# Kernel tuning notes

Hardware: AMD Instinct MI355X
Metric: run time of the kernel (lower is better)

The kernel has to match this reference:

```python
import jax, jax.numpy as jnp
import numpy as np

UNIT1 = 16384
UNITS = 3 * UNIT1          # self.units = unit1 * 3
INPUT_DIM = 15             # pinned by goal/color/pos/act segment lengths
BATCH = 2048


def _make_mask():
    """Reproduce the per-unit diagonal connectivity masks as a dense [UNITS, INPUT_DIM]
    0/1 matrix (the diagonal of each unit's s[u] matrix).
    Probabilities match np.random.randint thresholds in the original:
      group1 (u < unit1):        cols 0:3 -> 1, 3:6 -> P=2/5, 6:9 -> P=1/10, 9:15 -> 0
      group2 (unit1..2*unit1):   cols 0:3 -> P=5/10, 3:6 -> P=4/5, 6:9 -> P=3/5, 9:15 -> P=2/10
      group3 (2*unit1..3*unit1): cols 0:3 -> 0, 3:6 -> P=1/5, 6:9 -> 1, 9:15 -> 1
    """
    rng = np.random.default_rng(0)

    def block(n, specs):
        cols = []
        for width, p in specs:
            if p <= 0.0:
                cols.append(np.zeros((n, width), np.float32))
            elif p >= 1.0:
                cols.append(np.ones((n, width), np.float32))
            else:
                cols.append((rng.random((n, width)) < p).astype(np.float32))
        return np.concatenate(cols, axis=1)

    g1 = block(UNIT1, [(3, 1.0), (3, 0.4), (3, 0.1), (6, 0.0)])
    g2 = block(UNIT1, [(3, 0.5), (3, 0.8), (3, 0.6), (6, 0.2)])
    g3 = block(UNIT1, [(3, 0.0), (3, 0.2), (3, 1.0), (6, 1.0)])
    return np.concatenate([g1, g2, g3], axis=0)  # [UNITS, INPUT_DIM]


def setup_inputs() -> dict:
    key = jax.random.key(0)
    k_x, k_w = jax.random.split(key)
    inputs = jax.random.normal(k_x, (BATCH, INPUT_DIM), dtype=jnp.float32)
    # w_init = uniform(0, 0.01); non_neg constraint is satisfied at init
    w = jax.random.uniform(k_w, (INPUT_DIM, UNITS), dtype=jnp.float32,
                           minval=0.0, maxval=0.01)
    # b_init = uniform(0, 0) == zeros
    b = jnp.zeros((UNITS,), dtype=jnp.float32)
    mask = jnp.asarray(_make_mask())  # [UNITS, INPUT_DIM], structural constant
    return {"inputs": inputs, "w": w, "b": b, "mask": mask}


def reference(inputs, w, b, mask):
    # Original: p = (s @ inputs^T)^T -> [B, U, D]; f = diag(p @ w) + b -> [B, U].
    # Since s[u] = diag(mask[u]):
    #   f[b, u] = sum_i inputs[b, i] * mask[u, i] * w[i, u] + b[u]
    # i.e. a dense GEMM with the elementwise-masked weight matrix.
    masked_w = w * mask.T                    # [D, U]
    return inputs @ masked_w + b             # [B, U]
```

## Files before the change

### kernel.cpp

```cpp
#include <hip/hip_runtime.h>

#define UNITS     49152
#define INPUT_DIM 15
#define BATCH     2048

constexpr int TPB            = 256;
constexpr int U_PER_THREAD   = 4;
constexpr int U_PER_BLOCK    = TPB * U_PER_THREAD;
constexpr int ROWS_PER_BLOCK = 32;

typedef float f32x4 __attribute__((ext_vector_type(4)));

__global__ __launch_bounds__(TPB) void premask_kernel(
    const float* __restrict__ w,
    const float* __restrict__ mask,
    float* __restrict__ mw)
{
    const int u = blockIdx.x * TPB + threadIdx.x;
    float m[INPUT_DIM];
#pragma unroll
    for (int i = 0; i < INPUT_DIM; ++i) m[i] = mask[(size_t)u * INPUT_DIM + i];
#pragma unroll
    for (int i = 0; i < INPUT_DIM; ++i)
        mw[(size_t)i * UNITS + u] = w[(size_t)i * UNITS + u] * m[i];
}

template <bool PREMASKED>
__global__ __launch_bounds__(TPB) void striatum_kernel(
    const float* __restrict__ x,
    const float* __restrict__ w,
    const float* __restrict__ bias,
    const float* __restrict__ mask,
    float* __restrict__ out)
{
    __shared__ float xs[ROWS_PER_BLOCK * INPUT_DIM];

    const int u0   = blockIdx.x * U_PER_BLOCK + threadIdx.x * U_PER_THREAD;
    const int row0 = blockIdx.y * ROWS_PER_BLOCK;

    for (int idx = threadIdx.x; idx < ROWS_PER_BLOCK * INPUT_DIM; idx += TPB) {
        xs[idx] = x[row0 * INPUT_DIM + idx];
    }

    f32x4 mw[INPUT_DIM];
#pragma unroll
    for (int i = 0; i < INPUT_DIM; ++i) {
        f32x4 wv = *reinterpret_cast<const f32x4*>(&w[(size_t)i * UNITS + u0]);
        if constexpr (!PREMASKED) {
            wv.x *= mask[(size_t)(u0 + 0) * INPUT_DIM + i];
            wv.y *= mask[(size_t)(u0 + 1) * INPUT_DIM + i];
            wv.z *= mask[(size_t)(u0 + 2) * INPUT_DIM + i];
            wv.w *= mask[(size_t)(u0 + 3) * INPUT_DIM + i];
        }
        mw[i] = wv;
    }
    const f32x4 bv = *reinterpret_cast<const f32x4*>(&bias[u0]);

    __syncthreads();

    for (int r = 0; r < ROWS_PER_BLOCK; ++r) {
        const float* xr = &xs[r * INPUT_DIM];
        f32x4 acc = bv;
#pragma unroll
        for (int i = 0; i < INPUT_DIM; ++i) {
            const float xv = xr[i];
            acc.x = fmaf(xv, mw[i].x, acc.x);
            acc.y = fmaf(xv, mw[i].y, acc.y);
            acc.z = fmaf(xv, mw[i].z, acc.z);
            acc.w = fmaf(xv, mw[i].w, acc.w);
        }
        *reinterpret_cast<f32x4*>(&out[(size_t)(row0 + r) * UNITS + u0]) = acc;
    }
}

extern "C" void kernel_launch(void* const* d_in, const int* in_sizes, int n_in,
                              void* d_out, int out_size, void* d_ws, size_t ws_size,
                              hipStream_t stream) {
    const float* x    = (const float*)d_in[0];
    const float* w    = (const float*)d_in[1];
    const float* b    = (const float*)d_in[2];
    const float* mask = (const float*)d_in[3];
    float* out        = (float*)d_out;

    dim3 grid(UNITS / U_PER_BLOCK, BATCH / ROWS_PER_BLOCK);
    const size_t mw_bytes = (size_t)INPUT_DIM * UNITS * sizeof(float);

    if (ws_size >= mw_bytes) {
        float* mw = (float*)d_ws;
        premask_kernel<<<UNITS / TPB, TPB, 0, stream>>>(w, mask, mw);
        striatum_kernel<true><<<grid, TPB, 0, stream>>>(x, mw, b, mask, out);
    } else {
        striatum_kernel<false><<<grid, TPB, 0, stream>>>(x, w, b, mask, out);
    }
}
```

Before: 86.91 us.

## Reshape grid to fewer larger blocks, vectorize x loads, nontemporal stores

Changes the block size to 384 threads and the grid to 32 column blocks by 8 row groups of 256 rows each, so every block reuses its register-resident masked weights across many more rows. The shared x tile is padded to a stride of 16 so rows can be read as float4, and four rows are processed per iteration. Output is written with nontemporal stores, since the output is a large write-only stream. The grid shrinks to 256 blocks, which may underfill the GPU's compute units and lengthen the per-block tail.

After: 94.40 us. 8.6% more time.

```diff
diff --git a/kernel.cpp b/kernel.cpp
--- a/kernel.cpp
+++ b/kernel.cpp
@@ -4,19 +4,23 @@
 #define INPUT_DIM 15
 #define BATCH     2048
 
-constexpr int TPB            = 256;
+constexpr int TPB            = 384;
 constexpr int U_PER_THREAD   = 4;
 constexpr int U_PER_BLOCK    = TPB * U_PER_THREAD;
-constexpr int ROWS_PER_BLOCK = 32;
+constexpr int COL_BLOCKS     = UNITS / U_PER_BLOCK;
+constexpr int ROW_GROUPS     = 8;
+constexpr int ROWS_PER_BLOCK = BATCH / ROW_GROUPS;
+constexpr int XS_STRIDE      = 16;
+constexpr int R_UNROLL       = 4;
 
 typedef float f32x4 __attribute__((ext_vector_type(4)));
 
-__global__ __launch_bounds__(TPB) void premask_kernel(
+__global__ __launch_bounds__(256) void premask_kernel(
     const float* __restrict__ w,
     const float* __restrict__ mask,
     float* __restrict__ mw)
 {
-    const int u = blockIdx.x * TPB + threadIdx.x;
+    const int u = blockIdx.x * 256 + threadIdx.x;
     float m[INPUT_DIM];
 #pragma unroll
     for (int i = 0; i < INPUT_DIM; ++i) m[i] = mask[(size_t)u * INPUT_DIM + i];
@@ -33,13 +37,14 @@
     const float* __restrict__ mask,
     float* __restrict__ out)
 {
-    __shared__ float xs[ROWS_PER_BLOCK * INPUT_DIM];
+    __shared__ __align__(16) float xs[ROWS_PER_BLOCK * XS_STRIDE];
 
     const int u0   = blockIdx.x * U_PER_BLOCK + threadIdx.x * U_PER_THREAD;
     const int row0 = blockIdx.y * ROWS_PER_BLOCK;
 
-    for (int idx = threadIdx.x; idx < ROWS_PER_BLOCK * INPUT_DIM; idx += TPB) {
-        xs[idx] = x[row0 * INPUT_DIM + idx];
+    for (int idx = threadIdx.x; idx < ROWS_PER_BLOCK * XS_STRIDE; idx += TPB) {
+        const int row = idx >> 4, col = idx & 15;
+        xs[idx] = (col < INPUT_DIM) ? x[(size_t)(row0 + row) * INPUT_DIM + col] : 0.0f;
     }
 
     f32x4 mw[INPUT_DIM];
@@ -58,18 +63,39 @@
 
     __syncthreads();
 
-    for (int r = 0; r < ROWS_PER_BLOCK; ++r) {
-        const float* xr = &xs[r * INPUT_DIM];
-        f32x4 acc = bv;
+    const f32x4* xs4 = reinterpret_cast<const f32x4*>(xs);
+
+    for (int r = 0; r < ROWS_PER_BLOCK; r += R_UNROLL) {
+        float v[R_UNROLL][16];
+#pragma unroll
+        for (int rr = 0; rr < R_UNROLL; ++rr) {
+#pragma unroll
+            for (int j = 0; j < 4; ++j) {
+                const f32x4 t = xs4[(r + rr) * 4 + j];
+                v[rr][j * 4 + 0] = t.x;
+                v[rr][j * 4 + 1] = t.y;
+                v[rr][j * 4 + 2] = t.z;
+                v[rr][j * 4 + 3] = t.w;
+            }
+        }
+        f32x4 acc[R_UNROLL];
+#pragma unroll
+        for (int rr = 0; rr < R_UNROLL; ++rr) acc[rr] = bv;
 #pragma unroll
         for (int i = 0; i < INPUT_DIM; ++i) {
-            const float xv = xr[i];
-            acc.x = fmaf(xv, mw[i].x, acc.x);
-            acc.y = fmaf(xv, mw[i].y, acc.y);
-            acc.z = fmaf(xv, mw[i].z, acc.z);
-            acc.w = fmaf(xv, mw[i].w, acc.w);
+#pragma unroll
+            for (int rr = 0; rr < R_UNROLL; ++rr) {
+                acc[rr].x = fmaf(v[rr][i], mw[i].x, acc[rr].x);
+                acc[rr].y = fmaf(v[rr][i], mw[i].y, acc[rr].y);
+                acc[rr].z = fmaf(v[rr][i], mw[i].z, acc[rr].z);
+                acc[rr].w = fmaf(v[rr][i], mw[i].w, acc[rr].w);
+            }
         }
-        *reinterpret_cast<f32x4*>(&out[(size_t)(row0 + r) * UNITS + u0]) = acc;
+#pragma unroll
+        for (int rr = 0; rr < R_UNROLL; ++rr) {
+            __builtin_nontemporal_store(acc[rr],
+                reinterpret_cast<f32x4*>(&out[(size_t)(row0 + r + rr) * UNITS + u0]));
+        }
     }
 }
 
@@ -82,12 +108,12 @@
     const float* mask = (const float*)d_in[3];
     float* out        = (float*)d_out;
 
-    dim3 grid(UNITS / U_PER_BLOCK, BATCH / ROWS_PER_BLOCK);
+    dim3 grid(COL_BLOCKS, ROW_GROUPS);
     const size_t mw_bytes = (size_t)INPUT_DIM * UNITS * sizeof(float);
 
     if (ws_size >= mw_bytes) {
         float* mw = (float*)d_ws;
-        premask_kernel<<<UNITS / TPB, TPB, 0, stream>>>(w, mask, mw);
+        premask_kernel<<<UNITS / 256, 256, 0, stream>>>(w, mask, mw);
         striatum_kernel<true><<<grid, TPB, 0, stream>>>(x, mw, b, mask, out);
     } else {
         striatum_kernel<false><<<grid, TPB, 0, stream>>>(x, w, b, mask, out);
```
